# Kernel optimization log

Hardware: AMD Instinct MI355X
Metric: run time of the kernel (lower is better)

The kernel has to match this reference:

```python
import jax, jax.numpy as jnp
import numpy as np

SMOOTH = 1e-6
ALPHA = 0.25
GAMMA = 2.0
W_DICE, W_CLDICE, W_FOCAL = 0.1, 0.7, 0.2


def _shift(x, dy, dx):
    # x: [B,H,W]; value of neighbor at (i+dy, j+dx), zero-padded borders
    H, W = x.shape[1], x.shape[2]
    p = jnp.pad(x, ((0, 0), (1, 1), (1, 1)))
    return p[:, 1 + dy:1 + dy + H, 1 + dx:1 + dx + W]


def _thin_subiter(img, sub):
    # One Zhang-Suen thinning sub-iteration (matches skimage 2D skeletonize algorithm).
    p2 = _shift(img, -1, 0)   # N
    p3 = _shift(img, -1, 1)   # NE
    p4 = _shift(img, 0, 1)    # E
    p5 = _shift(img, 1, 1)    # SE
    p6 = _shift(img, 1, 0)    # S
    p7 = _shift(img, 1, -1)   # SW
    p8 = _shift(img, 0, -1)   # W
    p9 = _shift(img, -1, -1)  # NW
    nbrs = [p2, p3, p4, p5, p6, p7, p8, p9]
    B = sum(nbrs)
    # A = number of 0->1 transitions in circular sequence p2..p9
    A = sum(((nbrs[k] < 0.5) & (nbrs[(k + 1) % 8] > 0.5)).astype(jnp.int32)
            for k in range(8))
    c1 = (B >= 2.0) & (B <= 6.0)
    c2 = (A == 1)
    if sub == 0:
        c3 = (p2 * p4 * p6) == 0.0
        c4 = (p4 * p6 * p8) == 0.0
    else:
        c3 = (p2 * p4 * p8) == 0.0
        c4 = (p2 * p6 * p8) == 0.0
    remove = (img > 0.5) & c1 & c2 & c3 & c4
    return jnp.where(remove, 0.0, img)


def _skeletonize(img):
    # img: [B,H,W] float32 in {0,1}. Iterate thinning to convergence.
    def body(state):
        cur, _ = state
        new = _thin_subiter(_thin_subiter(cur, 0), 1)
        return (new, jnp.any(new != cur))

    out, _ = jax.lax.while_loop(lambda s: s[1], body, (img, jnp.array(True)))
    return out


def setup_inputs() -> dict:
    key = jax.random.key(0)
    k1, k2 = jax.random.split(key)
    logits = jax.random.normal(k1, (16, 2, 512, 512), dtype=jnp.float32)
    true = jax.random.randint(k2, (16, 512, 512), 0, 2, dtype=jnp.int32)
    return {"logits": logits, "true": true}


def reference(logits, true):
    probs = jax.nn.softmax(logits, axis=1)

    # --- clDice (detached in torch original -> stop_gradient, non-differentiable) ---
    pred = jax.lax.stop_gradient(probs[:, 1])          # [B,H,W]
    pred_bin = (pred > 0.5).astype(jnp.float32)
    true_bin = (true > 0).astype(jnp.float32)
    pred_skel = _skeletonize(pred_bin)
    true_skel = _skeletonize(true_bin)
    inter = jnp.sum(pred_skel * true_skel, axis=(1, 2))
    denom = jnp.sum(pred_skel, axis=(1, 2)) + jnp.sum(true_skel, axis=(1, 2))
    cldice = (2.0 * inter + SMOOTH) / (denom + SMOOTH)
    cldice_loss = 1.0 - jnp.mean(cldice)

    # --- Dice ---
    n_cls = probs.shape[1]
    t1h = jax.nn.one_hot(true, n_cls, axis=1, dtype=probs.dtype)  # [B,C,H,W]
    inter_d = jnp.sum(probs * t1h, axis=(0, 2, 3))
    card = jnp.sum(probs + t1h, axis=(0, 2, 3))
    dice_loss = 1.0 - jnp.mean((2.0 * inter_d + SMOOTH) / (card + SMOOTH))

    # --- Focal ---
    logp = jax.nn.log_softmax(logits, axis=1)
    ce = -jnp.take_along_axis(logp, true[:, None, :, :].astype(jnp.int32), axis=1)[:, 0]
    pt = jnp.exp(-ce)
    focal_loss = jnp.mean(ALPHA * (1.0 - pt) ** GAMMA * ce)

    return W_CLDICE * cldice_loss + W_DICE * dice_loss + W_FOCAL * focal_loss
```

## Files before the change

kernel.cpp:

```cpp
#include <hip/hip_runtime.h>
#include <hip/hip_bf16.h>

typedef unsigned long long u64;

#define NB 16
#define HW 512
#define PIX_PER_B (HW * HW)
#define NPIX (NB * PIX_PER_B)
#define WORDS_PER_B (PIX_PER_B / 64)
#define SROW 9

#define K1_BLOCKS 512
#define WS_PART_OFF 1024
#define WS_MASK_OFF 32768
#define WS_NEED_MASKS (WS_MASK_OFF + (size_t)2 * NB * WORDS_PER_B * 8)


__device__ __forceinline__ void fa3(u64 a, u64 b, u64 c, u64& s, u64& cy) {
  u64 x = a ^ b;
  s = x ^ c;
  cy = (a & b) | (c & x);
}

__device__ __forceinline__ u64 thin_word(u64 nm, u64 nl, u64 nr,
                                         u64 cm, u64 cl, u64 cr,
                                         u64 sm, u64 sl, u64 sr, int sub) {
  u64 p2 = nm;
  u64 p3 = (nm >> 1) | (nr << 63);
  u64 p4 = (cm >> 1) | (cr << 63);
  u64 p5 = (sm >> 1) | (sr << 63);
  u64 p6 = sm;
  u64 p7 = (sm << 1) | (sl >> 63);
  u64 p8 = (cm << 1) | (cl >> 63);
  u64 p9 = (nm << 1) | (nl >> 63);

  u64 u1, v1, u2, v2, ss, sc, cs, cc;
  fa3(p2, p3, p4, u1, v1);
  fa3(p5, p6, p7, u2, v2);
  u64 u3 = p8 ^ p9, v3 = p8 & p9;
  fa3(u1, u2, u3, ss, sc);
  fa3(v1, v2, v3, cs, cc);
  u64 w  = sc & cs;
  u64 b1 = sc ^ cs;
  u64 b2 = cc ^ w;
  u64 b3 = cc & w;
  u64 cond1 = (sc | cs | cc) & ~(b3 | (b2 & b1 & ss));

  u64 t0 = ~p2 & p3, t1 = ~p3 & p4, t2 = ~p4 & p5, t3 = ~p5 & p6;
  u64 t4 = ~p6 & p7, t5 = ~p7 & p8, t6 = ~p8 & p9, t7 = ~p9 & p2;
  u64 as1, ac1, as2, ac2, Ass, Asc, Acs, Acc;
  fa3(t0, t1, t2, as1, ac1);
  fa3(t3, t4, t5, as2, ac2);
  u64 as3 = t6 ^ t7, ac3 = t6 & t7;
  fa3(as1, as2, as3, Ass, Asc);
  fa3(ac1, ac2, ac3, Acs, Acc);
  u64 cond2 = Ass & ~(Asc | Acs | Acc);

  u64 cond3, cond4;
  if (sub == 0) { cond3 = ~(p2 & p4 & p6); cond4 = ~(p4 & p6 & p8); }
  else          { cond3 = ~(p2 & p4 & p8); cond4 = ~(p2 & p6 & p8); }

  u64 rem = cm & cond1 & cond2 & cond3 & cond4;
  return cm & ~rem;
}


__global__ __launch_bounds__(256) void loss_reduce_kernel(
    const float* __restrict__ logits, const int* __restrict__ tr,
    unsigned char* __restrict__ ws, int writeMasks) {
  int tid = threadIdx.x;
  double a0 = 0, a1 = 0, s0 = 0, s1 = 0, cnt = 0, fo = 0;
  u64* predM = (u64*)(ws + WS_MASK_OFF);
  u64* trueM = predM + (size_t)NB * WORDS_PER_B;

  const int iters = NPIX / (K1_BLOCKS * 256);
  for (int it = 0; it < iters; ++it) {
    int g = (it * K1_BLOCKS + (int)blockIdx.x) * 256 + tid;
    int b = g >> 18;
    int r = g & (PIX_PER_B - 1);
    const float* lp = logits + (size_t)b * 2 * PIX_PER_B + r;
    float l0 = lp[0], l1 = lp[PIX_PER_B];
    int t = tr[g];
    float m = fmaxf(l0, l1);
    float e0 = expf(l0 - m), e1 = expf(l1 - m);
    float s = e0 + e1;
    float p0 = e0 / s, p1 = e1 / s;
    if (t) a1 += (double)p1; else a0 += (double)p0;
    s0 += (double)p0;
    s1 += (double)p1;
    cnt += (double)t;
    float lse = m + logf(s);
    float ce = lse - (t ? l1 : l0);
    float pt = t ? p1 : p0;
    float om = 1.0f - pt;
    fo += (double)(0.25f * om * om * ce);
    if (writeMasks) {
      u64 pm = __ballot(p1 > 0.5f);
      u64 tm = __ballot(t > 0);
      if ((tid & 63) == 0) { predM[g >> 6] = pm; trueM[g >> 6] = tm; }
    }
  }

  __shared__ double red[4][6];
  double v[6] = {a0, a1, s0, s1, cnt, fo};
  int lane = tid & 63, wv = tid >> 6;
#pragma unroll
  for (int j = 0; j < 6; j++) {
    double x = v[j];
    for (int o = 32; o; o >>= 1) x += __shfl_down(x, o, 64);
    if (lane == 0) red[wv][j] = x;
  }
  __syncthreads();
  if (tid < 6) {
    double* part = (double*)(ws + WS_PART_OFF) + (size_t)blockIdx.x * 6;
    part[tid] = red[0][tid] + red[1][tid] + red[2][tid] + red[3][tid];
  }
}


__global__ __launch_bounds__(1024) void skel_split_kernel(unsigned char* __restrict__ ws) {
  __shared__ u64 S[HW * SROW];
  __shared__ unsigned char dirty[2][130];
  __shared__ int flag;

  int tid  = threadIdx.x;
  int b    = blockIdx.x;
  int img  = b & 15;
  int wcol = tid & 7;
  int s    = tid >> 3;
  int r0   = s * 4;
  int lane = tid & 63;

  u64* region = (u64*)(ws + WS_MASK_OFF) + (size_t)b * WORDS_PER_B;
  u64* clSp = (u64*)(ws + 192);
  u64* clSt = (u64*)(ws + 320);

#pragma unroll
  for (int i = 0; i < 4; i++)
    S[(r0 + i) * SROW + wcol] = region[(r0 + i) * 8 + wcol];
  if (tid < 130) {
    unsigned char init = (tid >= 1 && tid <= 128) ? 1 : 0;
    dirty[0][tid] = init;
    dirty[1][tid] = init;
  }
  if (tid == 0) flag = 0;
  __syncthreads();

  auto loadRow = [&](int r, u64& m, u64& l, u64& rr) {
    if (r < 0 || r >= HW) { m = 0; l = 0; rr = 0; return; }
    const u64* row = &S[r * SROW];
    m  = row[wcol];
    l  = wcol ? row[wcol - 1] : 0ULL;
    rr = (wcol < 7) ? row[wcol + 1] : 0ULL;
  };

  auto subIter = [&](int sub, int db, int pairTag) {
    unsigned char* dOut = dirty[db ^ 1];
    bool laneActive = (dirty[0][s] | dirty[0][s + 1] | dirty[0][s + 2] |
                       dirty[1][s] | dirty[1][s + 1] | dirty[1][s + 2]) != 0;
    u64 wmask = __ballot(laneActive);
    bool stripCh = false;
    u64 nw[4];
    bool doit = (wmask != 0);
    if (doit) {
      u64 am, al, ar, bm, bl, br, cmv, clv, crv, oldc[4];
      loadRow(r0 - 1, am, al, ar);
      loadRow(r0,     bm, bl, br);
#pragma unroll
      for (int i = 0; i < 4; i++) {
        loadRow(r0 + 1 + i, cmv, clv, crv);
        oldc[i] = bm;
        nw[i] = thin_word(am, al, ar, bm, bl, br, cmv, clv, crv, sub);
        am = bm; al = bl; ar = br;
        bm = cmv; bl = clv; br = crv;
      }
      bool ch = false;
#pragma unroll
      for (int i = 0; i < 4; i++) ch |= (nw[i] != oldc[i]);
      u64 bal = __ballot(ch);
      stripCh = ((bal >> (lane & 56)) & 0xFFULL) != 0;
    }
    __syncthreads();
    if (doit) {
#pragma unroll
      for (int i = 0; i < 4; i++) S[(r0 + i) * SROW + wcol] = nw[i];
    }
    if ((tid & 7) == 0) {
      dOut[s + 1] = stripCh ? 1 : 0;
      if (stripCh) flag = pairTag;
    }
    __syncthreads();
  };

  for (int pair = 1; pair <= 2000; ++pair) {
    subIter(0, 0, pair);
    subIter(1, 1, pair);
    if (flag != pair) break;
  }

  u64 cnt = 0;
#pragma unroll
  for (int i = 0; i < 4; i++) {
    u64 w = S[(r0 + i) * SROW + wcol];
    region[(r0 + i) * 8 + wcol] = w;
    cnt += (u64)__popcll(w);
  }
  for (int o = 32; o; o >>= 1) cnt += __shfl_down(cnt, o, 64);
  if (lane == 0) atomicAdd((b < NB ? clSp : clSt) + img, cnt);
}


__global__ __launch_bounds__(1024) void skel_combined_kernel(
    const float* __restrict__ logits, const int* __restrict__ tr,
    unsigned char* __restrict__ ws) {
  __shared__ u64 S[HW * SROW];
  __shared__ int flag;

  int tid  = threadIdx.x;
  int b    = blockIdx.x;
  int wcol = tid & 7;
  int r0   = (tid >> 3) * 4;
  int lane = tid & 63;

  u64* clInter = (u64*)(ws + 64);
  u64* clSp    = (u64*)(ws + 192);
  u64* clSt    = (u64*)(ws + 320);

  auto buildPredCompute = [&]() {
    const float* lp0 = logits + (size_t)b * 2 * PIX_PER_B;
    const float* lp1 = lp0 + PIX_PER_B;
    for (int k = 0; k < PIX_PER_B / 1024; k++) {
      int p = k * 1024 + tid;
      float l0 = lp0[p], l1 = lp1[p];
      float m = fmaxf(l0, l1);
      float e0 = expf(l0 - m), e1 = expf(l1 - m);
      float p1v = e1 / (e0 + e1);
      u64 msk = __ballot(p1v > 0.5f);
      if (lane == 0) { int wi = p >> 6; S[(wi >> 3) * SROW + (wi & 7)] = msk; }
    }
    __syncthreads();
  };
  auto buildTrueCompute = [&]() {
    const int* tp = tr + (size_t)b * PIX_PER_B;
    for (int k = 0; k < PIX_PER_B / 1024; k++) {
      int p = k * 1024 + tid;
      u64 msk = __ballot(tp[p] > 0);
      if (lane == 0) { int wi = p >> 6; S[(wi >> 3) * SROW + (wi & 7)] = msk; }
    }
    __syncthreads();
  };

  auto loadRow = [&](int r, u64& m, u64& l, u64& rr) {
    if (r < 0 || r >= HW) { m = 0; l = 0; rr = 0; return; }
    const u64* row = &S[r * SROW];
    m  = row[wcol];
    l  = wcol ? row[wcol - 1] : 0ULL;
    rr = (wcol < 7) ? row[wcol + 1] : 0ULL;
  };

  auto subIter = [&](int sub) {
    u64 am, al, ar, bm, bl, br, cmv, clv, crv;
    u64 nw[4], oldc[4];
    loadRow(r0 - 1, am, al, ar);
    loadRow(r0,     bm, bl, br);
#pragma unroll
    for (int i = 0; i < 4; i++) {
      loadRow(r0 + 1 + i, cmv, clv, crv);
      oldc[i] = bm;
      nw[i] = thin_word(am, al, ar, bm, bl, br, cmv, clv, crv, sub);
      am = bm; al = bl; ar = br;
      bm = cmv; bl = clv; br = crv;
    }
    __syncthreads();
    bool ch = false;
#pragma unroll
    for (int i = 0; i < 4; i++) {
      S[(r0 + i) * SROW + wcol] = nw[i];
      ch |= (nw[i] != oldc[i]);
    }
    if (ch) flag = 1;
    __syncthreads();
  };

  auto thinConverge = [&]() {
    for (int it = 0; it < 2000; ++it) {
      if (tid == 0) flag = 0;
      __syncthreads();
      subIter(0);
      subIter(1);
      int f = flag;
      __syncthreads();
      if (!f) break;
    }
  };

  buildPredCompute();
  thinConverge();
  u64 pr[4];
  u64 spL = 0;
#pragma unroll
  for (int i = 0; i < 4; i++) {
    pr[i] = S[(r0 + i) * SROW + wcol];
    spL += (u64)__popcll(pr[i]);
  }
  __syncthreads();

  buildTrueCompute();
  thinConverge();
  u64 stL = 0, inL = 0;
#pragma unroll
  for (int i = 0; i < 4; i++) {
    u64 tw = S[(r0 + i) * SROW + wcol];
    stL += (u64)__popcll(tw);
    inL += (u64)__popcll(tw & pr[i]);
  }

  for (int o = 32; o; o >>= 1) {
    spL += __shfl_down(spL, o, 64);
    stL += __shfl_down(stL, o, 64);
    inL += __shfl_down(inL, o, 64);
  }
  if (lane == 0) {
    atomicAdd(clSp + b, spL);
    atomicAdd(clSt + b, stL);
    atomicAdd(clInter + b, inL);
  }
}


__global__ __launch_bounds__(256) void inter_kernel(unsigned char* __restrict__ ws) {
  int i = blockIdx.x;
  int tid = threadIdx.x;
  const u64* p = (const u64*)(ws + WS_MASK_OFF) + (size_t)i * WORDS_PER_B;
  const u64* t = p + (size_t)NB * WORDS_PER_B;
  u64 acc = 0;
  for (int w = tid; w < WORDS_PER_B; w += 256) acc += (u64)__popcll(p[w] & t[w]);
  for (int o = 32; o; o >>= 1) acc += __shfl_down(acc, o, 64);
  __shared__ u64 r[4];
  if ((tid & 63) == 0) r[tid >> 6] = acc;
  __syncthreads();
  if (tid == 0) {
    u64* clInter = (u64*)(ws + 64);
    clInter[i] = r[0] + r[1] + r[2] + r[3];
  }
}


__global__ __launch_bounds__(512) void finalize_kernel(unsigned char* __restrict__ ws,
                                                       float* __restrict__ out) {
  int tid = threadIdx.x;
  const double* part = (const double*)(ws + WS_PART_OFF);
  double v[6];
#pragma unroll
  for (int j = 0; j < 6; j++) v[j] = part[(size_t)tid * 6 + j];

  __shared__ double red[8][6];
  int lane = tid & 63, wv = tid >> 6;
#pragma unroll
  for (int j = 0; j < 6; j++) {
    double x = v[j];
    for (int o = 32; o; o >>= 1) x += __shfl_down(x, o, 64);
    if (lane == 0) red[wv][j] = x;
  }
  __syncthreads();
  if (tid == 0) {
    double t[6] = {0, 0, 0, 0, 0, 0};
    for (int w = 0; w < 8; w++)
      for (int j = 0; j < 6; j++) t[j] += red[w][j];
    double a0 = t[0], a1 = t[1], s0 = t[2], s1 = t[3], cnt = t[4], fo = t[5];

    const double N = (double)NPIX;
    double cnt0 = N - cnt;
    double card0 = s0 + cnt0, card1 = s1 + cnt;
    double dice = 0.5 * ((2.0 * a0 + 1e-6) / (card0 + 1e-6) +
                         (2.0 * a1 + 1e-6) / (card1 + 1e-6));
    double diceL = 1.0 - dice;
    double focalL = fo / N;

    const u64* clInter = (const u64*)(ws + 64);
    const u64* clSp    = (const u64*)(ws + 192);
    const u64* clSt    = (const u64*)(ws + 320);
    double cs = 0;
    for (int b = 0; b < NB; b++) {
      double inter = (double)clInter[b];
      double den = (double)(clSp[b] + clSt[b]);
      cs += (2.0 * inter + 1e-6) / (den + 1e-6);
    }
    double clL = 1.0 - cs / (double)NB;

    out[0] = (float)(0.7 * clL + 0.1 * diceL + 0.2 * focalL);
  }
}


extern "C" void kernel_launch(void* const* d_in, const int* in_sizes, int n_in,
                              void* d_out, int out_size, void* d_ws, size_t ws_size,
                              hipStream_t stream) {
  const float* logits = (const float*)d_in[0];
  const int* tr = (const int*)d_in[1];
  float* out = (float*)d_out;
  unsigned char* ws = (unsigned char*)d_ws;

  int useMasks = (ws_size >= WS_NEED_MASKS) ? 1 : 0;

  hipMemsetAsync(d_ws, 0, 512, stream);

  hipLaunchKernelGGL(loss_reduce_kernel, dim3(K1_BLOCKS), dim3(256), 0, stream,
                     logits, tr, ws, useMasks);
  if (useMasks) {
    hipLaunchKernelGGL(skel_split_kernel, dim3(2 * NB), dim3(1024), 0, stream, ws);
    hipLaunchKernelGGL(inter_kernel, dim3(NB), dim3(256), 0, stream, ws);
  } else {
    hipLaunchKernelGGL(skel_combined_kernel, dim3(NB), dim3(1024), 0, stream,
                       logits, tr, ws);
  }
  hipLaunchKernelGGL(finalize_kernel, dim3(1), dim3(512), 0, stream, ws, out);
}
```

Before: 144.6 us.

## Overlap loss reduction with skeletonization in one fused launch

Splits the old first pass into a light mask-only kernel that compares logits directly instead of computing softmax. A fused kernel then runs the 32 skeleton-thinning blocks next to 224 loss-reduction blocks, so the long serial thinning loop overlaps with the bandwidth-bound softmax/dice/focal reduction. The memset is replaced by in-kernel zeroing of the counters. The logits and labels are now read twice (once for masks, once for the reduction), and the l1>l0 test may differ from p1>0.5 in rare rounding cases.

```diff
diff --git a/kernel.cpp b/kernel.cpp
--- a/kernel.cpp
+++ b/kernel.cpp
@@ -10,10 +10,12 @@
 #define WORDS_PER_B (PIX_PER_B / 64)
 #define SROW 9
 
-#define K1_BLOCKS 512
 #define WS_PART_OFF 1024
 #define WS_MASK_OFF 32768
 #define WS_NEED_MASKS (WS_MASK_OFF + (size_t)2 * NB * WORDS_PER_B * 8)
+
+#define RED_BLOCKS 224
+#define FB_BLOCKS 512
 
 
 __device__ __forceinline__ void fa3(u64 a, u64 b, u64 c, u64& s, u64& cy) {
@@ -65,17 +67,239 @@
 }
 
 
-__global__ __launch_bounds__(256) void loss_reduce_kernel(
+__global__ __launch_bounds__(256) void mask_kernel(
     const float* __restrict__ logits, const int* __restrict__ tr,
-    unsigned char* __restrict__ ws, int writeMasks) {
+    unsigned char* __restrict__ ws) {
+  int tid = threadIdx.x, blk = blockIdx.x;
+  u64* predM = (u64*)(ws + WS_MASK_OFF);
+  u64* trueM = predM + (size_t)NB * WORDS_PER_B;
+  if (blk == 0 && tid < 56) ((u64*)(ws + 64))[tid] = 0;
+#pragma unroll 4
+  for (int it = 0; it < 64; ++it) {
+    int g = (it * 256 + blk) * 256 + tid;
+    int b = g >> 18;
+    int r = g & (PIX_PER_B - 1);
+    const float* lp = logits + (size_t)b * 2 * PIX_PER_B + r;
+    float l0 = lp[0], l1 = lp[PIX_PER_B];
+    int t = tr[g];
+    u64 pm = __ballot(l1 > l0);
+    u64 tm = __ballot(t > 0);
+    if ((tid & 63) == 0) { predM[g >> 6] = pm; trueM[g >> 6] = tm; }
+  }
+}
+
+
+__global__ __launch_bounds__(1024) void fused_kernel(
+    const float* __restrict__ logits, const int* __restrict__ tr,
+    unsigned char* __restrict__ ws) {
+  __shared__ u64 S[HW * SROW];
+  __shared__ unsigned char dirty[2][130];
+  __shared__ int flag;
+  __shared__ double red[16][6];
+
+  int tid  = threadIdx.x;
+  int lane = tid & 63;
+
+  if (blockIdx.x < 32) {
+    int b    = blockIdx.x;
+    int img  = b & 15;
+    int wcol = tid & 7;
+    int s    = tid >> 3;
+    int r0   = s * 4;
+
+    u64* region = (u64*)(ws + WS_MASK_OFF) + (size_t)b * WORDS_PER_B;
+    u64* clSp = (u64*)(ws + 192);
+    u64* clSt = (u64*)(ws + 320);
+
+#pragma unroll
+    for (int i = 0; i < 4; i++)
+      S[(r0 + i) * SROW + wcol] = region[(r0 + i) * 8 + wcol];
+    if (tid < 130) {
+      unsigned char init = (tid >= 1 && tid <= 128) ? 1 : 0;
+      dirty[0][tid] = init;
+      dirty[1][tid] = init;
+    }
+    if (tid == 0) flag = 0;
+    __syncthreads();
+
+    auto loadRow = [&](int r, u64& m, u64& l, u64& rr) {
+      if (r < 0 || r >= HW) { m = 0; l = 0; rr = 0; return; }
+      const u64* row = &S[r * SROW];
+      m  = row[wcol];
+      l  = wcol ? row[wcol - 1] : 0ULL;
+      rr = (wcol < 7) ? row[wcol + 1] : 0ULL;
+    };
+
+    auto subIter = [&](int sub, int db, int pairTag) {
+      unsigned char* dOut = dirty[db ^ 1];
+      bool laneActive = (dirty[0][s] | dirty[0][s + 1] | dirty[0][s + 2] |
+                         dirty[1][s] | dirty[1][s + 1] | dirty[1][s + 2]) != 0;
+      u64 wmask = __ballot(laneActive);
+      bool stripCh = false;
+      u64 nw[4];
+      bool doit = (wmask != 0);
+      if (doit) {
+        u64 am, al, ar, bm, bl, br, cmv, clv, crv, oldc[4];
+        loadRow(r0 - 1, am, al, ar);
+        loadRow(r0,     bm, bl, br);
+#pragma unroll
+        for (int i = 0; i < 4; i++) {
+          loadRow(r0 + 1 + i, cmv, clv, crv);
+          oldc[i] = bm;
+          nw[i] = thin_word(am, al, ar, bm, bl, br, cmv, clv, crv, sub);
+          am = bm; al = bl; ar = br;
+          bm = cmv; bl = clv; br = crv;
+        }
+        bool ch = false;
+#pragma unroll
+        for (int i = 0; i < 4; i++) ch |= (nw[i] != oldc[i]);
+        u64 bal = __ballot(ch);
+        stripCh = ((bal >> (lane & 56)) & 0xFFULL) != 0;
+      }
+      __syncthreads();
+      if (doit) {
+#pragma unroll
+        for (int i = 0; i < 4; i++) S[(r0 + i) * SROW + wcol] = nw[i];
+      }
+      if ((tid & 7) == 0) {
+        dOut[s + 1] = stripCh ? 1 : 0;
+        if (stripCh) flag = pairTag;
+      }
+      __syncthreads();
+    };
+
+    for (int pair = 1; pair <= 2000; ++pair) {
+      subIter(0, 0, pair);
+      subIter(1, 1, pair);
+      if (flag != pair) break;
+    }
+
+    u64 cnt = 0;
+#pragma unroll
+    for (int i = 0; i < 4; i++) {
+      u64 w = S[(r0 + i) * SROW + wcol];
+      region[(r0 + i) * 8 + wcol] = w;
+      cnt += (u64)__popcll(w);
+    }
+    for (int o = 32; o; o >>= 1) cnt += __shfl_down(cnt, o, 64);
+    if (lane == 0) atomicAdd((b < NB ? clSp : clSt) + img, cnt);
+
+  } else {
+    int rb = blockIdx.x - 32;
+    double a0 = 0, a1 = 0, s0 = 0, s1 = 0, cnt = 0, fo = 0;
+    for (int g = rb * 1024 + tid; g < NPIX; g += RED_BLOCKS * 1024) {
+      int b = g >> 18;
+      int r = g & (PIX_PER_B - 1);
+      const float* lp = logits + (size_t)b * 2 * PIX_PER_B + r;
+      float l0 = lp[0], l1 = lp[PIX_PER_B];
+      int t = tr[g];
+      float m = fmaxf(l0, l1);
+      float e0 = expf(l0 - m), e1 = expf(l1 - m);
+      float ssum = e0 + e1;
+      float p0 = e0 / ssum, p1 = e1 / ssum;
+      if (t) a1 += (double)p1; else a0 += (double)p0;
+      s0 += (double)p0;
+      s1 += (double)p1;
+      cnt += (double)t;
+      float lse = m + logf(ssum);
+      float ce = lse - (t ? l1 : l0);
+      float pt = t ? p1 : p0;
+      float om = 1.0f - pt;
+      fo += (double)(0.25f * om * om * ce);
+    }
+    double v[6] = {a0, a1, s0, s1, cnt, fo};
+    int wv = tid >> 6;
+#pragma unroll
+    for (int j = 0; j < 6; j++) {
+      double x = v[j];
+      for (int o = 32; o; o >>= 1) x += __shfl_down(x, o, 64);
+      if (lane == 0) red[wv][j] = x;
+    }
+    __syncthreads();
+    if (tid < 6) {
+      double t6 = 0;
+      for (int w = 0; w < 16; w++) t6 += red[w][tid];
+      double* part = (double*)(ws + WS_PART_OFF) + (size_t)rb * 6;
+      part[tid] = t6;
+    }
+  }
+}
+
+
+__global__ __launch_bounds__(256) void inter_kernel(unsigned char* __restrict__ ws) {
+  int i = blockIdx.x;
+  int tid = threadIdx.x;
+  const u64* p = (const u64*)(ws + WS_MASK_OFF) + (size_t)i * WORDS_PER_B;
+  const u64* t = p + (size_t)NB * WORDS_PER_B;
+  u64 acc = 0;
+  for (int w = tid; w < WORDS_PER_B; w += 256) acc += (u64)__popcll(p[w] & t[w]);
+  for (int o = 32; o; o >>= 1) acc += __shfl_down(acc, o, 64);
+  __shared__ u64 r[4];
+  if ((tid & 63) == 0) r[tid >> 6] = acc;
+  __syncthreads();
+  if (tid == 0) {
+    u64* clInter = (u64*)(ws + 64);
+    clInter[i] = r[0] + r[1] + r[2] + r[3];
+  }
+}
+
+
+__global__ __launch_bounds__(512) void finalize_kernel(unsigned char* __restrict__ ws,
+                                                       float* __restrict__ out, int count) {
+  int tid = threadIdx.x;
+  const double* part = (const double*)(ws + WS_PART_OFF);
+  double v[6] = {0, 0, 0, 0, 0, 0};
+  if (tid < count) {
+#pragma unroll
+    for (int j = 0; j < 6; j++) v[j] = part[(size_t)tid * 6 + j];
+  }
+  __shared__ double red[8][6];
+  int lane = tid & 63, wv = tid >> 6;
+#pragma unroll
+  for (int j = 0; j < 6; j++) {
+    double x = v[j];
+    for (int o = 32; o; o >>= 1) x += __shfl_down(x, o, 64);
+    if (lane == 0) red[wv][j] = x;
+  }
+  __syncthreads();
+  if (tid == 0) {
+    double t[6] = {0, 0, 0, 0, 0, 0};
+    for (int w = 0; w < 8; w++)
+      for (int j = 0; j < 6; j++) t[j] += red[w][j];
+    double a0 = t[0], a1 = t[1], s0 = t[2], s1 = t[3], cnt = t[4], fo = t[5];
+
+    const double N = (double)NPIX;
+    double cnt0 = N - cnt;
+    double card0 = s0 + cnt0, card1 = s1 + cnt;
+    double dice = 0.5 * ((2.0 * a0 + 1e-6) / (card0 + 1e-6) +
+                         (2.0 * a1 + 1e-6) / (card1 + 1e-6));
+    double diceL = 1.0 - dice;
+    double focalL = fo / N;
+
+    const u64* clInter = (const u64*)(ws + 64);
+    const u64* clSp    = (const u64*)(ws + 192);
+    const u64* clSt    = (const u64*)(ws + 320);
+    double cs = 0;
+    for (int b = 0; b < NB; b++) {
+      double inter = (double)clInter[b];
+      double den = (double)(clSp[b] + clSt[b]);
+      cs += (2.0 * inter + 1e-6) / (den + 1e-6);
+    }
+    double clL = 1.0 - cs / (double)NB;
+
+    out[0] = (float)(0.7 * clL + 0.1 * diceL + 0.2 * focalL);
+  }
+}
+
+
+__global__ __launch_bounds__(256) void loss_reduce_fb_kernel(
+    const float* __restrict__ logits, const int* __restrict__ tr,
+    unsigned char* __restrict__ ws) {
   int tid = threadIdx.x;
   double a0 = 0, a1 = 0, s0 = 0, s1 = 0, cnt = 0, fo = 0;
-  u64* predM = (u64*)(ws + WS_MASK_OFF);
-  u64* trueM = predM + (size_t)NB * WORDS_PER_B;
-
-  const int iters = NPIX / (K1_BLOCKS * 256);
+  const int iters = NPIX / (FB_BLOCKS * 256);
   for (int it = 0; it < iters; ++it) {
-    int g = (it * K1_BLOCKS + (int)blockIdx.x) * 256 + tid;
+    int g = (it * FB_BLOCKS + (int)blockIdx.x) * 256 + tid;
     int b = g >> 18;
     int r = g & (PIX_PER_B - 1);
     const float* lp = logits + (size_t)b * 2 * PIX_PER_B + r;
@@ -94,13 +318,7 @@
     float pt = t ? p1 : p0;
     float om = 1.0f - pt;
     fo += (double)(0.25f * om * om * ce);
-    if (writeMasks) {
-      u64 pm = __ballot(p1 > 0.5f);
-      u64 tm = __ballot(t > 0);
-      if ((tid & 63) == 0) { predM[g >> 6] = pm; trueM[g >> 6] = tm; }
-    }
-  }
-
+  }
   __shared__ double red[4][6];
   double v[6] = {a0, a1, s0, s1, cnt, fo};
   int lane = tid & 63, wv = tid >> 6;
@@ -116,99 +334,6 @@
     part[tid] = red[0][tid] + red[1][tid] + red[2][tid] + red[3][tid];
   }
 }
-
-
-__global__ __launch_bounds__(1024) void skel_split_kernel(unsigned char* __restrict__ ws) {
-  __shared__ u64 S[HW * SROW];
-  __shared__ unsigned char dirty[2][130];
-  __shared__ int flag;
-
-  int tid  = threadIdx.x;
-  int b    = blockIdx.x;
-  int img  = b & 15;
-  int wcol = tid & 7;
-  int s    = tid >> 3;
-  int r0   = s * 4;
-  int lane = tid & 63;
-
-  u64* region = (u64*)(ws + WS_MASK_OFF) + (size_t)b * WORDS_PER_B;
-  u64* clSp = (u64*)(ws + 192);
-  u64* clSt = (u64*)(ws + 320);
-
-#pragma unroll
-  for (int i = 0; i < 4; i++)
-    S[(r0 + i) * SROW + wcol] = region[(r0 + i) * 8 + wcol];
-  if (tid < 130) {
-    unsigned char init = (tid >= 1 && tid <= 128) ? 1 : 0;
-    dirty[0][tid] = init;
-    dirty[1][tid] = init;
-  }
-  if (tid == 0) flag = 0;
-  __syncthreads();
-
-  auto loadRow = [&](int r, u64& m, u64& l, u64& rr) {
-    if (r < 0 || r >= HW) { m = 0; l = 0; rr = 0; return; }
-    const u64* row = &S[r * SROW];
-    m  = row[wcol];
-    l  = wcol ? row[wcol - 1] : 0ULL;
-    rr = (wcol < 7) ? row[wcol + 1] : 0ULL;
-  };
-
-  auto subIter = [&](int sub, int db, int pairTag) {
-    unsigned char* dOut = dirty[db ^ 1];
-    bool laneActive = (dirty[0][s] | dirty[0][s + 1] | dirty[0][s + 2] |
-                       dirty[1][s] | dirty[1][s + 1] | dirty[1][s + 2]) != 0;
-    u64 wmask = __ballot(laneActive);
-    bool stripCh = false;
-    u64 nw[4];
-    bool doit = (wmask != 0);
-    if (doit) {
-      u64 am, al, ar, bm, bl, br, cmv, clv, crv, oldc[4];
-      loadRow(r0 - 1, am, al, ar);
-      loadRow(r0,     bm, bl, br);
-#pragma unroll
-      for (int i = 0; i < 4; i++) {
-        loadRow(r0 + 1 + i, cmv, clv, crv);
-        oldc[i] = bm;
-        nw[i] = thin_word(am, al, ar, bm, bl, br, cmv, clv, crv, sub);
-        am = bm; al = bl; ar = br;
-        bm = cmv; bl = clv; br = crv;
-      }
-      bool ch = false;
-#pragma unroll
-      for (int i = 0; i < 4; i++) ch |= (nw[i] != oldc[i]);
-      u64 bal = __ballot(ch);
-      stripCh = ((bal >> (lane & 56)) & 0xFFULL) != 0;
-    }
-    __syncthreads();
-    if (doit) {
-#pragma unroll
-      for (int i = 0; i < 4; i++) S[(r0 + i) * SROW + wcol] = nw[i];
-    }
-    if ((tid & 7) == 0) {
-      dOut[s + 1] = stripCh ? 1 : 0;
-      if (stripCh) flag = pairTag;
-    }
-    __syncthreads();
-  };
-
-  for (int pair = 1; pair <= 2000; ++pair) {
-    subIter(0, 0, pair);
-    subIter(1, 1, pair);
-    if (flag != pair) break;
-  }
-
-  u64 cnt = 0;
-#pragma unroll
-  for (int i = 0; i < 4; i++) {
-    u64 w = S[(r0 + i) * SROW + wcol];
-    region[(r0 + i) * 8 + wcol] = w;
-    cnt += (u64)__popcll(w);
-  }
-  for (int o = 32; o; o >>= 1) cnt += __shfl_down(cnt, o, 64);
-  if (lane == 0) atomicAdd((b < NB ? clSp : clSt) + img, cnt);
-}
-
 
 __global__ __launch_bounds__(1024) void skel_combined_kernel(
     const float* __restrict__ logits, const int* __restrict__ tr,
@@ -226,21 +351,17 @@
   u64* clSp    = (u64*)(ws + 192);
   u64* clSt    = (u64*)(ws + 320);
 
-  auto buildPredCompute = [&]() {
+  auto buildPred = [&]() {
     const float* lp0 = logits + (size_t)b * 2 * PIX_PER_B;
     const float* lp1 = lp0 + PIX_PER_B;
     for (int k = 0; k < PIX_PER_B / 1024; k++) {
       int p = k * 1024 + tid;
-      float l0 = lp0[p], l1 = lp1[p];
-      float m = fmaxf(l0, l1);
-      float e0 = expf(l0 - m), e1 = expf(l1 - m);
-      float p1v = e1 / (e0 + e1);
-      u64 msk = __ballot(p1v > 0.5f);
+      u64 msk = __ballot(lp1[p] > lp0[p]);
       if (lane == 0) { int wi = p >> 6; S[(wi >> 3) * SROW + (wi & 7)] = msk; }
     }
     __syncthreads();
   };
-  auto buildTrueCompute = [&]() {
+  auto buildTrue = [&]() {
     const int* tp = tr + (size_t)b * PIX_PER_B;
     for (int k = 0; k < PIX_PER_B / 1024; k++) {
       int p = k * 1024 + tid;
@@ -294,7 +415,7 @@
     }
   };
 
-  buildPredCompute();
+  buildPred();
   thinConverge();
   u64 pr[4];
   u64 spL = 0;
@@ -305,7 +426,7 @@
   }
   __syncthreads();
 
-  buildTrueCompute();
+  buildTrue();
   thinConverge();
   u64 stL = 0, inL = 0;
 #pragma unroll
@@ -324,71 +445,6 @@
     atomicAdd(clSp + b, spL);
     atomicAdd(clSt + b, stL);
     atomicAdd(clInter + b, inL);
-  }
-}
-
-
-__global__ __launch_bounds__(256) void inter_kernel(unsigned char* __restrict__ ws) {
-  int i = blockIdx.x;
-  int tid = threadIdx.x;
-  const u64* p = (const u64*)(ws + WS_MASK_OFF) + (size_t)i * WORDS_PER_B;
-  const u64* t = p + (size_t)NB * WORDS_PER_B;
-  u64 acc = 0;
-  for (int w = tid; w < WORDS_PER_B; w += 256) acc += (u64)__popcll(p[w] & t[w]);
-  for (int o = 32; o; o >>= 1) acc += __shfl_down(acc, o, 64);
-  __shared__ u64 r[4];
-  if ((tid & 63) == 0) r[tid >> 6] = acc;
-  __syncthreads();
-  if (tid == 0) {
-    u64* clInter = (u64*)(ws + 64);
-    clInter[i] = r[0] + r[1] + r[2] + r[3];
-  }
-}
-
-
-__global__ __launch_bounds__(512) void finalize_kernel(unsigned char* __restrict__ ws,
-                                                       float* __restrict__ out) {
-  int tid = threadIdx.x;
-  const double* part = (const double*)(ws + WS_PART_OFF);
-  double v[6];
-#pragma unroll
-  for (int j = 0; j < 6; j++) v[j] = part[(size_t)tid * 6 + j];
-
-  __shared__ double red[8][6];
-  int lane = tid & 63, wv = tid >> 6;
-#pragma unroll
-  for (int j = 0; j < 6; j++) {
-    double x = v[j];
-    for (int o = 32; o; o >>= 1) x += __shfl_down(x, o, 64);
-    if (lane == 0) red[wv][j] = x;
-  }
-  __syncthreads();
-  if (tid == 0) {
-    double t[6] = {0, 0, 0, 0, 0, 0};
-    for (int w = 0; w < 8; w++)
-      for (int j = 0; j < 6; j++) t[j] += red[w][j];
-    double a0 = t[0], a1 = t[1], s0 = t[2], s1 = t[3], cnt = t[4], fo = t[5];
-
-    const double N = (double)NPIX;
-    double cnt0 = N - cnt;
-    double card0 = s0 + cnt0, card1 = s1 + cnt;
-    double dice = 0.5 * ((2.0 * a0 + 1e-6) / (card0 + 1e-6) +
-                         (2.0 * a1 + 1e-6) / (card1 + 1e-6));
-    double diceL = 1.0 - dice;
-    double focalL = fo / N;
-
-    const u64* clInter = (const u64*)(ws + 64);
-    const u64* clSp    = (const u64*)(ws + 192);
-    const u64* clSt    = (const u64*)(ws + 320);
-    double cs = 0;
-    for (int b = 0; b < NB; b++) {
-      double inter = (double)clInter[b];
-      double den = (double)(clSp[b] + clSt[b]);
-      cs += (2.0 * inter + 1e-6) / (den + 1e-6);
-    }
-    double clL = 1.0 - cs / (double)NB;
-
-    out[0] = (float)(0.7 * clL + 0.1 * diceL + 0.2 * focalL);
   }
 }
 
@@ -401,18 +457,18 @@
   float* out = (float*)d_out;
   unsigned char* ws = (unsigned char*)d_ws;
 
-  int useMasks = (ws_size >= WS_NEED_MASKS) ? 1 : 0;
-
-  hipMemsetAsync(d_ws, 0, 512, stream);
-
-  hipLaunchKernelGGL(loss_reduce_kernel, dim3(K1_BLOCKS), dim3(256), 0, stream,
-                     logits, tr, ws, useMasks);
-  if (useMasks) {
-    hipLaunchKernelGGL(skel_split_kernel, dim3(2 * NB), dim3(1024), 0, stream, ws);
+  if (ws_size >= WS_NEED_MASKS) {
+    hipLaunchKernelGGL(mask_kernel, dim3(256), dim3(256), 0, stream, logits, tr, ws);
+    hipLaunchKernelGGL(fused_kernel, dim3(32 + RED_BLOCKS), dim3(1024), 0, stream,
+                       logits, tr, ws);
     hipLaunchKernelGGL(inter_kernel, dim3(NB), dim3(256), 0, stream, ws);
+    hipLaunchKernelGGL(finalize_kernel, dim3(1), dim3(512), 0, stream, ws, out, RED_BLOCKS);
   } else {
+    hipMemsetAsync(d_ws, 0, 512, stream);
+    hipLaunchKernelGGL(loss_reduce_fb_kernel, dim3(FB_BLOCKS), dim3(256), 0, stream,
+                       logits, tr, ws);
     hipLaunchKernelGGL(skel_combined_kernel, dim3(NB), dim3(1024), 0, stream,
                        logits, tr, ws);
-  }
-  hipLaunchKernelGGL(finalize_kernel, dim3(1), dim3(512), 0, stream, ws, out);
-}
+    hipLaunchKernelGGL(finalize_kernel, dim3(1), dim3(512), 0, stream, ws, out, FB_BLOCKS);
+  }
+}
```

Measured after the change: 147.9 us. +2.3%, slower.
